# Optimization experiments

Hardware: AMD Instinct MI355X
Metric: run time of the kernel (lower is better)

The kernel has to match this reference:

```python
import jax, jax.numpy as jnp
import numpy as np

B, T, D = 2, 2048, 2048
N_HEADS, N_KV = 16, 4
HD = D // N_HEADS  # 128
ROPE_BASE = 10000.0


def _rope_tables(t, dim, base=ROPE_BASE):
    inv_freq = 1.0 / (base ** (jnp.arange(0, dim, 2, dtype=jnp.float32) / dim))
    freqs = jnp.arange(t, dtype=jnp.float32)[:, None] * inv_freq[None, :]  # (T, dim/2)
    emb = jnp.concatenate([freqs, freqs], axis=-1)  # (T, dim)
    return jnp.cos(emb), jnp.sin(emb)


def _rotate_half(x):
    x1, x2 = jnp.split(x, 2, axis=-1)
    return jnp.concatenate([-x2, x1], axis=-1)


def _apply_rope(x, cos, sin):
    # x: (B, H, T, hd); cos/sin: (T, hd)
    return x * cos[None, None] + _rotate_half(x) * sin[None, None]


def setup_inputs() -> dict:
    key = jax.random.key(0)
    ks = jax.random.split(key, 5)
    s = 0.02
    return {
        "x": jax.random.normal(ks[0], (B, T, D), jnp.float32),
        "wq": jax.random.normal(ks[1], (D, N_HEADS * HD), jnp.float32) * s,
        "wk": jax.random.normal(ks[2], (D, N_KV * HD), jnp.float32) * s,
        "wv": jax.random.normal(ks[3], (D, N_KV * HD), jnp.float32) * s,
        "wo": jax.random.normal(ks[4], (D, D), jnp.float32) * s,
    }


def reference(x, wq, wk, wv, wo):
    b, t, c = x.shape
    n_rep = N_HEADS // N_KV
    scale = 1.0 / np.sqrt(HD)

    q = (x @ wq).reshape(b, t, N_HEADS, HD).transpose(0, 2, 1, 3)  # (B,H,T,hd)
    k = (x @ wk).reshape(b, t, N_KV, HD).transpose(0, 2, 1, 3)     # (B,Hkv,T,hd)
    v = (x @ wv).reshape(b, t, N_KV, HD).transpose(0, 2, 1, 3)

    cos, sin = _rope_tables(t, HD)
    q = _apply_rope(q, cos, sin)
    k = _apply_rope(k, cos, sin)

    # repeat_kv (GQA)
    k = jnp.repeat(k, n_rep, axis=1)  # (B,H,T,hd)
    v = jnp.repeat(v, n_rep, axis=1)

    scores = jnp.einsum("bhqd,bhkd->bhqk", q, k) * scale
    causal = jnp.tril(jnp.ones((t, t), dtype=bool))
    scores = jnp.where(causal[None, None], scores, -jnp.inf)
    attn = jax.nn.softmax(scores, axis=-1)
    out = jnp.einsum("bhqk,bhkd->bhqd", attn, v)
    out = out.transpose(0, 2, 1, 3).reshape(b, t, c)
    return out @ wo
```

## Files before the change

kernel.cpp:

```cpp
#include <hip/hip_runtime.h>
#include <hip/hip_bf16.h>
#include <math.h>

#define B_   2
#define T_   2048
#define D_   2048
#define NH_  16
#define NKV_ 4
#define HD_  128
#define MROWS (B_*T_)
#define NQKV  (NH_*HD_ + 2*NKV_*HD_)

typedef __bf16 bf16_t;
typedef __bf16 bf16x8 __attribute__((ext_vector_type(8)));
typedef __bf16 bf16x4 __attribute__((ext_vector_type(4)));
typedef float  floatx4 __attribute__((ext_vector_type(4)));

__device__ __forceinline__ void async_copy16(const bf16_t* gsrc, bf16_t* ldst) {
  __builtin_amdgcn_global_load_lds(
      (const __attribute__((address_space(1))) unsigned int*)gsrc,
      (__attribute__((address_space(3))) unsigned int*)ldst, 16, 0, 0);
}

__global__ void prep_fused(const float* __restrict__ s0, const float* __restrict__ s1,
                           const float* __restrict__ s2, const float* __restrict__ s3,
                           const float* __restrict__ sx,
                           bf16_t* __restrict__ d0, bf16_t* __restrict__ d1,
                           bf16_t* __restrict__ d2, bf16_t* __restrict__ d3,
                           bf16_t* __restrict__ dx) {
  const int z = blockIdx.z;
  const int tx = threadIdx.x, ty = threadIdx.y;
  if (z == 4) {
    int i = ((blockIdx.y * 64 + blockIdx.x) * 256 + ty * 32 + tx) * 8;
    float4 a = *(const float4*)(sx + i);
    float4 b = *(const float4*)(sx + i + 4);
    bf16x8 v;
    v[0]=(bf16_t)a.x; v[1]=(bf16_t)a.y; v[2]=(bf16_t)a.z; v[3]=(bf16_t)a.w;
    v[4]=(bf16_t)b.x; v[5]=(bf16_t)b.y; v[6]=(bf16_t)b.z; v[7]=(bf16_t)b.w;
    *(bf16x8*)(dx + i) = v;
    return;
  }
  const int N = (z == 1 || z == 2) ? 512 : 2048;
  const int n0 = blockIdx.x * 32;
  if (n0 >= N) return;
  const float* src = (z == 0) ? s0 : (z == 1) ? s1 : (z == 2) ? s2 : s3;
  bf16_t*      dst = (z == 0) ? d0 : (z == 1) ? d1 : (z == 2) ? d2 : d3;
  const int K = 2048;
  __shared__ float tile[32][33];
  int k0 = blockIdx.y * 32;
#pragma unroll
  for (int r = 0; r < 4; r++)
    tile[ty + r*8][tx] = src[(size_t)(k0 + ty + r*8) * N + n0 + tx];
  __syncthreads();
#pragma unroll
  for (int r = 0; r < 4; r++)
    dst[(size_t)(n0 + ty + r*8) * K + k0 + tx] = (bf16_t)tile[tx][ty + r*8];
}

template <typename OUT_T>
__global__ __launch_bounds__(256, 3)
void gemm_bt(const bf16_t* __restrict__ A, const bf16_t* __restrict__ Bt,
             OUT_T* __restrict__ C, int M, int N, int K) {
  __shared__ __align__(16) bf16_t As[128 * 64];
  __shared__ __align__(16) bf16_t Bs[128 * 64];
  const int tid  = threadIdx.x;
  const int wave = tid >> 6, lane = tid & 63;
  const int quad = lane >> 4, l16 = lane & 15;
  const int nBlocksM = M >> 7;
  const int bm = blockIdx.x % nBlocksM, bn = blockIdx.x / nBlocksM;
  const int m0 = bm * 128, n0 = bn * 128;
  const int wm = (wave >> 1) * 64, wn = (wave & 1) * 64;

  floatx4 acc[4][4];
#pragma unroll
  for (int i = 0; i < 4; i++)
#pragma unroll
    for (int j = 0; j < 4; j++) acc[i][j] = floatx4{0.f, 0.f, 0.f, 0.f};

  for (int k0 = 0; k0 < K; k0 += 64) {
    __syncthreads();
#pragma unroll
    for (int i = 0; i < 4; i++) {
      int e = i * 256 + tid;
      int row = e >> 3, grp = e & 7;
      int gg = grp ^ (row & 7);
      async_copy16(A + (size_t)(m0 + row) * K + k0 + gg * 8, As + e * 8);
    }
#pragma unroll
    for (int i = 0; i < 4; i++) {
      int e = i * 256 + tid;
      int row = e >> 3, grp = e & 7;
      int gg = grp ^ (row & 7);
      async_copy16(Bt + (size_t)(n0 + row) * K + k0 + gg * 8, Bs + e * 8);
    }
    __syncthreads();
#pragma unroll
    for (int ks = 0; ks < 2; ks++) {
      bf16x8 af[4], bfr[4];
      int grp = ks * 4 + quad;
#pragma unroll
      for (int mi = 0; mi < 4; mi++) {
        int row = wm + mi * 16 + l16;
        af[mi] = *(const bf16x8*)(As + row * 64 + ((grp ^ (row & 7)) << 3));
      }
#pragma unroll
      for (int ni = 0; ni < 4; ni++) {
        int row = wn + ni * 16 + l16;
        bfr[ni] = *(const bf16x8*)(Bs + row * 64 + ((grp ^ (row & 7)) << 3));
      }
#pragma unroll
      for (int mi = 0; mi < 4; mi++)
#pragma unroll
        for (int ni = 0; ni < 4; ni++)
          acc[mi][ni] = __builtin_amdgcn_mfma_f32_16x16x32_bf16(af[mi], bfr[ni], acc[mi][ni], 0, 0, 0);
    }
  }
#pragma unroll
  for (int mi = 0; mi < 4; mi++) {
#pragma unroll
    for (int r = 0; r < 4; r++) {
      int row = m0 + wm + mi * 16 + quad * 4 + r;
      size_t base = (size_t)row * N + n0 + wn;
#pragma unroll
      for (int ni = 0; ni < 4; ni++)
        C[base + ni * 16 + l16] = (OUT_T)acc[mi][ni][r];
    }
  }
}

#define ROPE_BLOCKS ((MROWS * NKV_ * 64) / 256)
__global__ void kv_prep(const bf16_t* __restrict__ qkv, bf16_t* __restrict__ Kb,
                        bf16_t* __restrict__ Vt) {
  if (blockIdx.x < ROPE_BLOCKS) {
    int g = blockIdx.x * 256 + threadIdx.x;
    int j = g & 63;
    int rest = g >> 6;
    int kvh = rest & 3;
    int row = rest >> 2;
    int t = row & (T_ - 1);
    int b = row >> 11;
    const bf16_t* src = qkv + (size_t)row * NQKV + NH_ * HD_ + kvh * HD_;
    float ang = (float)t * __expf(-0.14391156816f * (float)j);
    float sn, cs;
    __sincosf(ang, &sn, &cs);
    float x0 = (float)src[j];
    float x1 = (float)src[j + 64];
    bf16_t* dst = Kb + ((size_t)(b * NKV_ + kvh) * T_ + t) * HD_;
    dst[j]      = (bf16_t)(x0 * cs - x1 * sn);
    dst[j + 64] = (bf16_t)(x1 * cs + x0 * sn);
    return;
  }
  __shared__ float tile[32][33];
  int bb = blockIdx.x - ROPE_BLOCKS;
  int bx = bb & 63, by = (bb >> 6) & 3, bz = bb >> 8;
  int t0 = bx * 32, d0 = by * 32;
  int b = bz / NKV_, kvh = bz % NKV_;
  int tx = threadIdx.x & 31, ty = threadIdx.x >> 5;
#pragma unroll
  for (int r = 0; r < 4; r++) {
    int t = t0 + ty + r * 8;
    tile[ty + r*8][tx] =
        (float)qkv[(size_t)(b * T_ + t) * NQKV + (NH_ + NKV_) * HD_ + kvh * HD_ + d0 + tx];
  }
  __syncthreads();
#pragma unroll
  for (int r = 0; r < 4; r++) {
    int d = d0 + ty + r * 8;
    Vt[((size_t)(b * NKV_ + kvh) * HD_ + d) * T_ + t0 + tx] = (bf16_t)tile[tx][ty + r*8];
  }
}

__global__ __launch_bounds__(256, 2)
void flash_attn(const bf16_t* __restrict__ qkv, const bf16_t* __restrict__ Kb,
                const bf16_t* __restrict__ Vt, bf16_t* __restrict__ Ob) {
  __shared__ __align__(16) bf16_t Ks[2][64 * 128];
  __shared__ __align__(16) bf16_t Vs[2][128 * 64];

  const int tid = threadIdx.x;
  const int wave = tid >> 6, lane = tid & 63;
  const int quad = lane >> 4, l16 = lane & 15;
  const int nQT = T_ / 64;
  const int bid = blockIdx.x;
  const int bh = bid % (B_ * NH_);
  const int qt = (nQT - 1) - (bid / (B_ * NH_));
  const int h = bh % NH_;
  const int b = bh / NH_;
  const int kv = h >> 2;

  const bf16_t* kbase = Kb + ((size_t)(b * NKV_ + kv) * T_) * HD_;
  const bf16_t* vbase = Vt + ((size_t)(b * NKV_ + kv) * HD_) * T_;

  auto stage = [&](int kt, int bufi) {
#pragma unroll
    for (int i = 0; i < 4; i++) {
      int e = i * 256 + tid;
      int row = e >> 4, grp = e & 15;
      int gg = grp ^ (row & 15);
      async_copy16(kbase + (size_t)(kt * 64 + row) * HD_ + gg * 8, &Ks[bufi][e * 8]);
    }
#pragma unroll
    for (int i = 0; i < 4; i++) {
      int e = i * 256 + tid;
      int row = e >> 3, grp = e & 7;
      int gg = grp ^ (row & 7);
      async_copy16(vbase + (size_t)row * T_ + kt * 64 + gg * 8, &Vs[bufi][e * 8]);
    }
  };

  stage(0, 0);

  bf16x8 qf[4];
  {
    const int t_row = qt * 64 + wave * 16 + l16;
    const bf16_t* qptr = qkv + (size_t)(b * T_ + t_row) * NQKV + h * HD_;
    bf16x8 qraw[4];
#pragma unroll
    for (int ks = 0; ks < 4; ks++)
      qraw[ks] = *(const bf16x8*)(qptr + ks * 32 + quad * 8);
    const float scale = 0.12751651541057752f;
#pragma unroll
    for (int ks = 0; ks < 2; ks++)
#pragma unroll
      for (int j = 0; j < 8; j++) {
        int d = ks * 32 + quad * 8 + j;
        float ang = (float)t_row * __expf(-0.14391156816f * (float)d);
        float sn, cs;
        __sincosf(ang, &sn, &cs);
        float lo = (float)qraw[ks][j], hi = (float)qraw[ks + 2][j];
        qf[ks][j]     = (bf16_t)((lo * cs - hi * sn) * scale);
        qf[ks + 2][j] = (bf16_t)((hi * cs + lo * sn) * scale);
      }
  }

  floatx4 o[8];
#pragma unroll
  for (int i = 0; i < 8; i++) o[i] = floatx4{0.f, 0.f, 0.f, 0.f};
  float m_s = -1e30f, l_s = 0.f;

  for (int kt = 0; kt <= qt; kt++) {
    const int bufi = kt & 1;
    __syncthreads();
    if (kt < qt) stage(kt + 1, bufi ^ 1);

    floatx4 s[4];
#pragma unroll
    for (int nt = 0; nt < 4; nt++) s[nt] = floatx4{0.f, 0.f, 0.f, 0.f};
    __builtin_amdgcn_s_setprio(1);
#pragma unroll
    for (int ks = 0; ks < 4; ks++) {
      int grp = ks * 4 + quad;
#pragma unroll
      for (int nt = 0; nt < 4; nt++) {
        int row = nt * 16 + l16;
        bf16x8 kf = *(const bf16x8*)(&Ks[bufi][row * 128 + ((grp ^ (row & 15)) << 3)]);
        s[nt] = __builtin_amdgcn_mfma_f32_16x16x32_bf16(kf, qf[ks], s[nt], 0, 0, 0);
      }
    }
    __builtin_amdgcn_s_setprio(0);

    if (kt == qt) {
      int qlocal = wave * 16 + l16;
#pragma unroll
      for (int nt = 0; nt < 4; nt++)
#pragma unroll
        for (int r = 0; r < 4; r++) {
          int klocal = nt * 16 + quad * 4 + r;
          if (klocal > qlocal) s[nt][r] = -1e30f;
        }
    }

    float mx = fmaxf(fmaxf(s[0][0], s[0][1]), fmaxf(s[0][2], s[0][3]));
#pragma unroll
    for (int nt = 1; nt < 4; nt++)
      mx = fmaxf(mx, fmaxf(fmaxf(s[nt][0], s[nt][1]), fmaxf(s[nt][2], s[nt][3])));
    mx = fmaxf(mx, __shfl_xor(mx, 16, 64));
    mx = fmaxf(mx, __shfl_xor(mx, 32, 64));
    if (!__all(mx <= m_s + 8.0f)) {
      float mnew = fmaxf(m_s, mx);
      float alpha = __builtin_amdgcn_exp2f(m_s - mnew);
      m_s = mnew;
      l_s *= alpha;
#pragma unroll
      for (int dt = 0; dt < 8; dt++) o[dt] *= alpha;
    }
    float sum = 0.f;
#pragma unroll
    for (int nt = 0; nt < 4; nt++)
#pragma unroll
      for (int r = 0; r < 4; r++) {
        float p = __builtin_amdgcn_exp2f(s[nt][r] - m_s);
        s[nt][r] = p;
        sum += p;
      }
    sum += __shfl_xor(sum, 16, 64);
    sum += __shfl_xor(sum, 32, 64);
    l_s += sum;

    __builtin_amdgcn_s_setprio(1);
#pragma unroll
    for (int ks = 0; ks < 2; ks++) {
      bf16x8 pf;
#pragma unroll
      for (int j = 0; j < 4; j++) {
        pf[j]     = (bf16_t)s[ks][j];
        pf[j + 4] = (bf16_t)s[ks + 2][j];
      }
      const int glo = 2 * ks + (quad >> 1);
      const int ghi = glo + 4;
      const int half = (quad & 1) * 4;
#pragma unroll
      for (int dt = 0; dt < 8; dt++) {
        int row = dt * 16 + l16;
        int sw = row & 7;
        const bf16_t* vrow = &Vs[bufi][row * 64];
        bf16x4 vlo = *(const bf16x4*)(vrow + (((glo ^ sw) << 3) + half));
        bf16x4 vhi = *(const bf16x4*)(vrow + (((ghi ^ sw) << 3) + half));
        bf16x8 vf = __builtin_shufflevector(vlo, vhi, 0, 1, 2, 3, 4, 5, 6, 7);
        o[dt] = __builtin_amdgcn_mfma_f32_16x16x32_bf16(vf, pf, o[dt], 0, 0, 0);
      }
    }
    __builtin_amdgcn_s_setprio(0);
  }

  {
    int qg = qt * 64 + wave * 16 + l16;
    float inv_l = 1.f / l_s;
    size_t base = ((size_t)(b * T_) + qg) * D_ + h * HD_;
#pragma unroll
    for (int dt = 0; dt < 8; dt++) {
      bf16x4 w;
#pragma unroll
      for (int r = 0; r < 4; r++) w[r] = (bf16_t)(o[dt][r] * inv_l);
      *(bf16x4*)(Ob + base + dt * 16 + quad * 4) = w;
    }
  }
}

extern "C" void kernel_launch(void* const* d_in, const int* in_sizes, int n_in,
                              void* d_out, int out_size, void* d_ws, size_t ws_size,
                              hipStream_t stream) {
  const float* x  = (const float*)d_in[0];
  const float* wq = (const float*)d_in[1];
  const float* wk = (const float*)d_in[2];
  const float* wv = (const float*)d_in[3];
  const float* wo = (const float*)d_in[4];
  float* out = (float*)d_out;

  bf16_t* x_bf   = (bf16_t*)d_ws;
  bf16_t* attn_o = x_bf;
  bf16_t* wqkv_t = x_bf + (size_t)MROWS * D_;
  bf16_t* wo_t   = wqkv_t + (size_t)NQKV * D_;
  bf16_t* qkv    = wo_t + (size_t)D_ * D_;
  bf16_t* Kb     = qkv + (size_t)MROWS * NQKV;
  bf16_t* Vt     = Kb + (size_t)B_ * NKV_ * T_ * HD_;

  prep_fused<<<dim3(64, 64, 5), dim3(32, 8), 0, stream>>>(
      wq, wk, wv, wo, x,
      wqkv_t, wqkv_t + (size_t)2048 * D_, wqkv_t + (size_t)2560 * D_, wo_t, x_bf);

  gemm_bt<bf16_t><<<(MROWS / 128) * (NQKV / 128), 256, 0, stream>>>(
      x_bf, wqkv_t, qkv, MROWS, NQKV, D_);

  kv_prep<<<ROPE_BLOCKS + (T_ / 32) * (HD_ / 32) * B_ * NKV_, 256, 0, stream>>>(
      qkv, Kb, Vt);

  flash_attn<<<B_ * NH_ * (T_ / 64), 256, 0, stream>>>(qkv, Kb, Vt, attn_o);

  gemm_bt<float><<<(MROWS / 128) * (D_ / 128), 256, 0, stream>>>(
      attn_o, wo_t, out, MROWS, D_, D_);
}
```

Measured before the change: 286.0 us.

## Process two query tiles per flash-attention block and pre-permute V layout

Each flash-attention workgroup now handles 128 query rows as two 64-row groups, so every K/V tile staged into LDS feeds twice as many MFMAs and global K/V traffic is halved. The V transpose in kv_prep writes keys in a permuted order so the PV MFMA operand can be read with one 16-byte LDS load instead of two 8-byte loads plus a shuffle. The grid is halved and the block order pairs long and short causal tiles. The cost is doubled accumulator and score register pressure under launch_bounds(256,2), which may cause spills or lower occupancy, plus some extra masked work on the last two key tiles.

```diff
diff --git a/kernel.cpp b/kernel.cpp
--- a/kernel.cpp
+++ b/kernel.cpp
@@ -166,7 +166,11 @@
 #pragma unroll
   for (int r = 0; r < 4; r++) {
     int d = d0 + ty + r * 8;
-    Vt[((size_t)(b * NKV_ + kvh) * HD_ + d) * T_ + t0 + tx] = (bf16_t)tile[tx][ty + r*8];
+    int t = t0 + tx;
+    int k = t & 63;
+    int pos = ((((k >> 4) & 1) * 4 + ((k >> 2) & 3)) << 3) + ((k >> 5) << 2) + (k & 3);
+    Vt[((size_t)(b * NKV_ + kvh) * HD_ + d) * T_ + (t & ~63) + pos] =
+        (bf16_t)tile[tx][ty + r*8];
   }
 }
 
@@ -179,13 +183,15 @@
   const int tid = threadIdx.x;
   const int wave = tid >> 6, lane = tid & 63;
   const int quad = lane >> 4, l16 = lane & 15;
-  const int nQT = T_ / 64;
   const int bid = blockIdx.x;
-  const int bh = bid % (B_ * NH_);
-  const int qt = (nQT - 1) - (bid / (B_ * NH_));
-  const int h = bh % NH_;
-  const int b = bh / NH_;
+  const int bh = bid & 31;
+  const int qtp = bid >> 5;
+  const int qt2 = (qtp < 8) ? (15 - qtp) : (qtp - 8);
+  const int h = bh & 15;
+  const int b = bh >> 4;
   const int kv = h >> 2;
+  const int q0 = qt2 * 128;
+  const int ktLast = 2 * qt2 + 1;
 
   const bf16_t* kbase = Kb + ((size_t)(b * NKV_ + kv) * T_) * HD_;
   const bf16_t* vbase = Vt + ((size_t)(b * NKV_ + kv) * HD_) * T_;
@@ -209,9 +215,10 @@
 
   stage(0, 0);
 
-  bf16x8 qf[4];
-  {
-    const int t_row = qt * 64 + wave * 16 + l16;
+  bf16x8 qf[2][4];
+#pragma unroll
+  for (int g = 0; g < 2; g++) {
+    const int t_row = q0 + g * 64 + wave * 16 + l16;
     const bf16_t* qptr = qkv + (size_t)(b * T_ + t_row) * NQKV + h * HD_;
     bf16x8 qraw[4];
 #pragma unroll
@@ -227,24 +234,30 @@
         float sn, cs;
         __sincosf(ang, &sn, &cs);
         float lo = (float)qraw[ks][j], hi = (float)qraw[ks + 2][j];
-        qf[ks][j]     = (bf16_t)((lo * cs - hi * sn) * scale);
-        qf[ks + 2][j] = (bf16_t)((hi * cs + lo * sn) * scale);
-      }
-  }
-
-  floatx4 o[8];
-#pragma unroll
-  for (int i = 0; i < 8; i++) o[i] = floatx4{0.f, 0.f, 0.f, 0.f};
-  float m_s = -1e30f, l_s = 0.f;
-
-  for (int kt = 0; kt <= qt; kt++) {
+        qf[g][ks][j]     = (bf16_t)((lo * cs - hi * sn) * scale);
+        qf[g][ks + 2][j] = (bf16_t)((hi * cs + lo * sn) * scale);
+      }
+  }
+
+  floatx4 o[2][8];
+#pragma unroll
+  for (int g = 0; g < 2; g++)
+#pragma unroll
+    for (int i = 0; i < 8; i++) o[g][i] = floatx4{0.f, 0.f, 0.f, 0.f};
+  float m_s[2] = {-1e30f, -1e30f}, l_s[2] = {0.f, 0.f};
+
+  const int qlocal64 = wave * 16 + l16;
+
+  for (int kt = 0; kt <= ktLast; kt++) {
     const int bufi = kt & 1;
     __syncthreads();
-    if (kt < qt) stage(kt + 1, bufi ^ 1);
-
-    floatx4 s[4];
-#pragma unroll
-    for (int nt = 0; nt < 4; nt++) s[nt] = floatx4{0.f, 0.f, 0.f, 0.f};
+    if (kt < ktLast) stage(kt + 1, bufi ^ 1);
+
+    floatx4 s[2][4];
+#pragma unroll
+    for (int g = 0; g < 2; g++)
+#pragma unroll
+      for (int nt = 0; nt < 4; nt++) s[g][nt] = floatx4{0.f, 0.f, 0.f, 0.f};
     __builtin_amdgcn_s_setprio(1);
 #pragma unroll
     for (int ks = 0; ks < 4; ks++) {
@@ -253,84 +266,91 @@
       for (int nt = 0; nt < 4; nt++) {
         int row = nt * 16 + l16;
         bf16x8 kf = *(const bf16x8*)(&Ks[bufi][row * 128 + ((grp ^ (row & 15)) << 3)]);
-        s[nt] = __builtin_amdgcn_mfma_f32_16x16x32_bf16(kf, qf[ks], s[nt], 0, 0, 0);
+        s[0][nt] = __builtin_amdgcn_mfma_f32_16x16x32_bf16(kf, qf[0][ks], s[0][nt], 0, 0, 0);
+        s[1][nt] = __builtin_amdgcn_mfma_f32_16x16x32_bf16(kf, qf[1][ks], s[1][nt], 0, 0, 0);
       }
     }
     __builtin_amdgcn_s_setprio(0);
 
-    if (kt == qt) {
-      int qlocal = wave * 16 + l16;
+#pragma unroll
+    for (int g = 0; g < 2; g++) {
+      int ktd = 2 * qt2 + g;
+      if (kt >= ktd) {
+        int koff = (kt - ktd) * 64;
+#pragma unroll
+        for (int nt = 0; nt < 4; nt++)
+#pragma unroll
+          for (int r = 0; r < 4; r++) {
+            int klocal = nt * 16 + quad * 4 + r + koff;
+            if (klocal > qlocal64) s[g][nt][r] = -1e30f;
+          }
+      }
+    }
+
+#pragma unroll
+    for (int g = 0; g < 2; g++) {
+      float mx = fmaxf(fmaxf(s[g][0][0], s[g][0][1]), fmaxf(s[g][0][2], s[g][0][3]));
+#pragma unroll
+      for (int nt = 1; nt < 4; nt++)
+        mx = fmaxf(mx, fmaxf(fmaxf(s[g][nt][0], s[g][nt][1]),
+                             fmaxf(s[g][nt][2], s[g][nt][3])));
+      mx = fmaxf(mx, __shfl_xor(mx, 16, 64));
+      mx = fmaxf(mx, __shfl_xor(mx, 32, 64));
+      if (!__all(mx <= m_s[g] + 8.0f)) {
+        float mnew = fmaxf(m_s[g], mx);
+        float alpha = __builtin_amdgcn_exp2f(m_s[g] - mnew);
+        m_s[g] = mnew;
+        l_s[g] *= alpha;
+#pragma unroll
+        for (int dt = 0; dt < 8; dt++) o[g][dt] *= alpha;
+      }
+      float sum = 0.f;
 #pragma unroll
       for (int nt = 0; nt < 4; nt++)
 #pragma unroll
         for (int r = 0; r < 4; r++) {
-          int klocal = nt * 16 + quad * 4 + r;
-          if (klocal > qlocal) s[nt][r] = -1e30f;
+          float p = __builtin_amdgcn_exp2f(s[g][nt][r] - m_s[g]);
+          s[g][nt][r] = p;
+          sum += p;
         }
-    }
-
-    float mx = fmaxf(fmaxf(s[0][0], s[0][1]), fmaxf(s[0][2], s[0][3]));
-#pragma unroll
-    for (int nt = 1; nt < 4; nt++)
-      mx = fmaxf(mx, fmaxf(fmaxf(s[nt][0], s[nt][1]), fmaxf(s[nt][2], s[nt][3])));
-    mx = fmaxf(mx, __shfl_xor(mx, 16, 64));
-    mx = fmaxf(mx, __shfl_xor(mx, 32, 64));
-    if (!__all(mx <= m_s + 8.0f)) {
-      float mnew = fmaxf(m_s, mx);
-      float alpha = __builtin_amdgcn_exp2f(m_s - mnew);
-      m_s = mnew;
-      l_s *= alpha;
-#pragma unroll
-      for (int dt = 0; dt < 8; dt++) o[dt] *= alpha;
-    }
-    float sum = 0.f;
-#pragma unroll
-    for (int nt = 0; nt < 4; nt++)
-#pragma unroll
-      for (int r = 0; r < 4; r++) {
-        float p = __builtin_amdgcn_exp2f(s[nt][r] - m_s);
-        s[nt][r] = p;
-        sum += p;
-      }
-    sum += __shfl_xor(sum, 16, 64);
-    sum += __shfl_xor(sum, 32, 64);
-    l_s += sum;
+      sum += __shfl_xor(sum, 16, 64);
+      sum += __shfl_xor(sum, 32, 64);
+      l_s[g] += sum;
+    }
 
     __builtin_amdgcn_s_setprio(1);
 #pragma unroll
     for (int ks = 0; ks < 2; ks++) {
-      bf16x8 pf;
+      bf16x8 pf0, pf1;
 #pragma unroll
       for (int j = 0; j < 4; j++) {
-        pf[j]     = (bf16_t)s[ks][j];
-        pf[j + 4] = (bf16_t)s[ks + 2][j];
-      }
-      const int glo = 2 * ks + (quad >> 1);
-      const int ghi = glo + 4;
-      const int half = (quad & 1) * 4;
+        pf0[j]     = (bf16_t)s[0][ks][j];
+        pf0[j + 4] = (bf16_t)s[0][ks + 2][j];
+        pf1[j]     = (bf16_t)s[1][ks][j];
+        pf1[j + 4] = (bf16_t)s[1][ks + 2][j];
+      }
+      const int G = ks * 4 + quad;
 #pragma unroll
       for (int dt = 0; dt < 8; dt++) {
         int row = dt * 16 + l16;
-        int sw = row & 7;
-        const bf16_t* vrow = &Vs[bufi][row * 64];
-        bf16x4 vlo = *(const bf16x4*)(vrow + (((glo ^ sw) << 3) + half));
-        bf16x4 vhi = *(const bf16x4*)(vrow + (((ghi ^ sw) << 3) + half));
-        bf16x8 vf = __builtin_shufflevector(vlo, vhi, 0, 1, 2, 3, 4, 5, 6, 7);
-        o[dt] = __builtin_amdgcn_mfma_f32_16x16x32_bf16(vf, pf, o[dt], 0, 0, 0);
+        bf16x8 vf = *(const bf16x8*)(&Vs[bufi][row * 64 + ((G ^ (row & 7)) << 3)]);
+        o[0][dt] = __builtin_amdgcn_mfma_f32_16x16x32_bf16(vf, pf0, o[0][dt], 0, 0, 0);
+        o[1][dt] = __builtin_amdgcn_mfma_f32_16x16x32_bf16(vf, pf1, o[1][dt], 0, 0, 0);
       }
     }
     __builtin_amdgcn_s_setprio(0);
   }
 
-  {
-    int qg = qt * 64 + wave * 16 + l16;
-    float inv_l = 1.f / l_s;
+#pragma unroll
+  for (int g = 0; g < 2; g++) {
+    int qg = q0 + g * 64 + wave * 16 + l16;
+    float inv_l = 1.f / l_s[g];
     size_t base = ((size_t)(b * T_) + qg) * D_ + h * HD_;
 #pragma unroll
     for (int dt = 0; dt < 8; dt++) {
       bf16x4 w;
 #pragma unroll
-      for (int r = 0; r < 4; r++) w[r] = (bf16_t)(o[dt][r] * inv_l);
+      for (int r = 0; r < 4; r++) w[r] = (bf16_t)(o[g][dt][r] * inv_l);
       *(bf16x4*)(Ob + base + dt * 16 + quad * 4) = w;
     }
   }
@@ -364,7 +384,7 @@
   kv_prep<<<ROPE_BLOCKS + (T_ / 32) * (HD_ / 32) * B_ * NKV_, 256, 0, stream>>>(
       qkv, Kb, Vt);
 
-  flash_attn<<<B_ * NH_ * (T_ / 64), 256, 0, stream>>>(qkv, Kb, Vt, attn_o);
+  flash_attn<<<B_ * NH_ * (T_ / 128), 256, 0, stream>>>(qkv, Kb, Vt, attn_o);
 
   gemm_bt<float><<<(MROWS / 128) * (D_ / 128), 256, 0, stream>>>(
       attn_o, wo_t, out, MROWS, D_, D_);
```

Result: no change. 284.4 us (-0.6%).

## Use 128-row query blocks sharing K/V tiles and pre-permute V layout

Applied to the files above, without the earlier changes.

Flash attention blocks now cover 128 query rows with 8 waves, so each staged K/V tile in LDS serves twice as many queries and staging per thread is halved. Work order is remapped so heavy and light causal tiles interleave. V is written in a permuted order during kv_prep so the PV step reads one 16-byte LDS vector instead of two 8-byte pieces plus a shuffle. The cost is that the lower-half waves sit idle on the final key tile, and the larger blocks may lower occupancy.

```diff
diff --git a/kernel.cpp b/kernel.cpp
--- a/kernel.cpp
+++ b/kernel.cpp
@@ -166,11 +166,15 @@
 #pragma unroll
   for (int r = 0; r < 4; r++) {
     int d = d0 + ty + r * 8;
-    Vt[((size_t)(b * NKV_ + kvh) * HD_ + d) * T_ + t0 + tx] = (bf16_t)tile[tx][ty + r*8];
-  }
-}
-
-__global__ __launch_bounds__(256, 2)
+    int t = t0 + tx;
+    int k = t & 63;
+    int pos = ((((k >> 4) & 1) * 4 + ((k >> 2) & 3)) << 3) + ((k >> 5) << 2) + (k & 3);
+    Vt[((size_t)(b * NKV_ + kvh) * HD_ + d) * T_ + (t & ~63) + pos] =
+        (bf16_t)tile[tx][ty + r*8];
+  }
+}
+
+__global__ __launch_bounds__(512, 4)
 void flash_attn(const bf16_t* __restrict__ qkv, const bf16_t* __restrict__ Kb,
                 const bf16_t* __restrict__ Vt, bf16_t* __restrict__ Ob) {
   __shared__ __align__(16) bf16_t Ks[2][64 * 128];
@@ -179,28 +183,32 @@
   const int tid = threadIdx.x;
   const int wave = tid >> 6, lane = tid & 63;
   const int quad = lane >> 4, l16 = lane & 15;
-  const int nQT = T_ / 64;
   const int bid = blockIdx.x;
-  const int bh = bid % (B_ * NH_);
-  const int qt = (nQT - 1) - (bid / (B_ * NH_));
-  const int h = bh % NH_;
-  const int b = bh / NH_;
+  const int bh = bid & 31;
+  const int p  = bid >> 5;
+  const int qm = (p < 8) ? (15 - p) : (p - 8);
+  const int h = bh & 15;
+  const int b = bh >> 4;
   const int kv = h >> 2;
+  const int wq = wave >> 2;
+  const int w4 = wave & 3;
+  const int qtw = 2 * qm + wq;
+  const int ktLast = 2 * qm + 1;
 
   const bf16_t* kbase = Kb + ((size_t)(b * NKV_ + kv) * T_) * HD_;
   const bf16_t* vbase = Vt + ((size_t)(b * NKV_ + kv) * HD_) * T_;
 
   auto stage = [&](int kt, int bufi) {
 #pragma unroll
-    for (int i = 0; i < 4; i++) {
-      int e = i * 256 + tid;
+    for (int i = 0; i < 2; i++) {
+      int e = i * 512 + tid;
       int row = e >> 4, grp = e & 15;
       int gg = grp ^ (row & 15);
       async_copy16(kbase + (size_t)(kt * 64 + row) * HD_ + gg * 8, &Ks[bufi][e * 8]);
     }
 #pragma unroll
-    for (int i = 0; i < 4; i++) {
-      int e = i * 256 + tid;
+    for (int i = 0; i < 2; i++) {
+      int e = i * 512 + tid;
       int row = e >> 3, grp = e & 7;
       int gg = grp ^ (row & 7);
       async_copy16(vbase + (size_t)row * T_ + kt * 64 + gg * 8, &Vs[bufi][e * 8]);
@@ -211,7 +219,7 @@
 
   bf16x8 qf[4];
   {
-    const int t_row = qt * 64 + wave * 16 + l16;
+    const int t_row = qtw * 64 + w4 * 16 + l16;
     const bf16_t* qptr = qkv + (size_t)(b * T_ + t_row) * NQKV + h * HD_;
     bf16x8 qraw[4];
 #pragma unroll
@@ -237,93 +245,90 @@
   for (int i = 0; i < 8; i++) o[i] = floatx4{0.f, 0.f, 0.f, 0.f};
   float m_s = -1e30f, l_s = 0.f;
 
-  for (int kt = 0; kt <= qt; kt++) {
+  const int qlocal = w4 * 16 + l16;
+
+  for (int kt = 0; kt <= ktLast; kt++) {
     const int bufi = kt & 1;
     __syncthreads();
-    if (kt < qt) stage(kt + 1, bufi ^ 1);
-
-    floatx4 s[4];
-#pragma unroll
-    for (int nt = 0; nt < 4; nt++) s[nt] = floatx4{0.f, 0.f, 0.f, 0.f};
-    __builtin_amdgcn_s_setprio(1);
-#pragma unroll
-    for (int ks = 0; ks < 4; ks++) {
-      int grp = ks * 4 + quad;
-#pragma unroll
-      for (int nt = 0; nt < 4; nt++) {
-        int row = nt * 16 + l16;
-        bf16x8 kf = *(const bf16x8*)(&Ks[bufi][row * 128 + ((grp ^ (row & 15)) << 3)]);
-        s[nt] = __builtin_amdgcn_mfma_f32_16x16x32_bf16(kf, qf[ks], s[nt], 0, 0, 0);
-      }
-    }
-    __builtin_amdgcn_s_setprio(0);
-
-    if (kt == qt) {
-      int qlocal = wave * 16 + l16;
+    if (kt < ktLast) stage(kt + 1, bufi ^ 1);
+
+    if (kt <= qtw) {
+      floatx4 s[4];
+#pragma unroll
+      for (int nt = 0; nt < 4; nt++) s[nt] = floatx4{0.f, 0.f, 0.f, 0.f};
+      __builtin_amdgcn_s_setprio(1);
+#pragma unroll
+      for (int ks = 0; ks < 4; ks++) {
+        int grp = ks * 4 + quad;
+#pragma unroll
+        for (int nt = 0; nt < 4; nt++) {
+          int row = nt * 16 + l16;
+          bf16x8 kf = *(const bf16x8*)(&Ks[bufi][row * 128 + ((grp ^ (row & 15)) << 3)]);
+          s[nt] = __builtin_amdgcn_mfma_f32_16x16x32_bf16(kf, qf[ks], s[nt], 0, 0, 0);
+        }
+      }
+      __builtin_amdgcn_s_setprio(0);
+
+      if (kt == qtw) {
+#pragma unroll
+        for (int nt = 0; nt < 4; nt++)
+#pragma unroll
+          for (int r = 0; r < 4; r++) {
+            int klocal = nt * 16 + quad * 4 + r;
+            if (klocal > qlocal) s[nt][r] = -1e30f;
+          }
+      }
+
+      float mx = fmaxf(fmaxf(s[0][0], s[0][1]), fmaxf(s[0][2], s[0][3]));
+#pragma unroll
+      for (int nt = 1; nt < 4; nt++)
+        mx = fmaxf(mx, fmaxf(fmaxf(s[nt][0], s[nt][1]), fmaxf(s[nt][2], s[nt][3])));
+      mx = fmaxf(mx, __shfl_xor(mx, 16, 64));
+      mx = fmaxf(mx, __shfl_xor(mx, 32, 64));
+      if (!__all(mx <= m_s + 8.0f)) {
+        float mnew = fmaxf(m_s, mx);
+        float alpha = __builtin_amdgcn_exp2f(m_s - mnew);
+        m_s = mnew;
+        l_s *= alpha;
+#pragma unroll
+        for (int dt = 0; dt < 8; dt++) o[dt] *= alpha;
+      }
+      float sum = 0.f;
 #pragma unroll
       for (int nt = 0; nt < 4; nt++)
 #pragma unroll
         for (int r = 0; r < 4; r++) {
-          int klocal = nt * 16 + quad * 4 + r;
-          if (klocal > qlocal) s[nt][r] = -1e30f;
+          float pv = __builtin_amdgcn_exp2f(s[nt][r] - m_s);
+          s[nt][r] = pv;
+          sum += pv;
         }
-    }
-
-    float mx = fmaxf(fmaxf(s[0][0], s[0][1]), fmaxf(s[0][2], s[0][3]));
-#pragma unroll
-    for (int nt = 1; nt < 4; nt++)
-      mx = fmaxf(mx, fmaxf(fmaxf(s[nt][0], s[nt][1]), fmaxf(s[nt][2], s[nt][3])));
-    mx = fmaxf(mx, __shfl_xor(mx, 16, 64));
-    mx = fmaxf(mx, __shfl_xor(mx, 32, 64));
-    if (!__all(mx <= m_s + 8.0f)) {
-      float mnew = fmaxf(m_s, mx);
-      float alpha = __builtin_amdgcn_exp2f(m_s - mnew);
-      m_s = mnew;
-      l_s *= alpha;
-#pragma unroll
-      for (int dt = 0; dt < 8; dt++) o[dt] *= alpha;
-    }
-    float sum = 0.f;
-#pragma unroll
-    for (int nt = 0; nt < 4; nt++)
-#pragma unroll
-      for (int r = 0; r < 4; r++) {
-        float p = __builtin_amdgcn_exp2f(s[nt][r] - m_s);
-        s[nt][r] = p;
-        sum += p;
-      }
-    sum += __shfl_xor(sum, 16, 64);
-    sum += __shfl_xor(sum, 32, 64);
-    l_s += sum;
-
-    __builtin_amdgcn_s_setprio(1);
-#pragma unroll
-    for (int ks = 0; ks < 2; ks++) {
-      bf16x8 pf;
-#pragma unroll
-      for (int j = 0; j < 4; j++) {
-        pf[j]     = (bf16_t)s[ks][j];
-        pf[j + 4] = (bf16_t)s[ks + 2][j];
-      }
-      const int glo = 2 * ks + (quad >> 1);
-      const int ghi = glo + 4;
-      const int half = (quad & 1) * 4;
-#pragma unroll
-      for (int dt = 0; dt < 8; dt++) {
-        int row = dt * 16 + l16;
-        int sw = row & 7;
-        const bf16_t* vrow = &Vs[bufi][row * 64];
-        bf16x4 vlo = *(const bf16x4*)(vrow + (((glo ^ sw) << 3) + half));
-        bf16x4 vhi = *(const bf16x4*)(vrow + (((ghi ^ sw) << 3) + half));
-        bf16x8 vf = __builtin_shufflevector(vlo, vhi, 0, 1, 2, 3, 4, 5, 6, 7);
-        o[dt] = __builtin_amdgcn_mfma_f32_16x16x32_bf16(vf, pf, o[dt], 0, 0, 0);
-      }
-    }
-    __builtin_amdgcn_s_setprio(0);
+      sum += __shfl_xor(sum, 16, 64);
+      sum += __shfl_xor(sum, 32, 64);
+      l_s += sum;
+
+      __builtin_amdgcn_s_setprio(1);
+#pragma unroll
+      for (int ks = 0; ks < 2; ks++) {
+        bf16x8 pf;
+#pragma unroll
+        for (int j = 0; j < 4; j++) {
+          pf[j]     = (bf16_t)s[ks][j];
+          pf[j + 4] = (bf16_t)s[ks + 2][j];
+        }
+        const int G = ks * 4 + quad;
+#pragma unroll
+        for (int dt = 0; dt < 8; dt++) {
+          int row = dt * 16 + l16;
+          bf16x8 vf = *(const bf16x8*)(&Vs[bufi][row * 64 + ((G ^ (row & 7)) << 3)]);
+          o[dt] = __builtin_amdgcn_mfma_f32_16x16x32_bf16(vf, pf, o[dt], 0, 0, 0);
+        }
+      }
+      __builtin_amdgcn_s_setprio(0);
+    }
   }
 
   {
-    int qg = qt * 64 + wave * 16 + l16;
+    int qg = qtw * 64 + w4 * 16 + l16;
     float inv_l = 1.f / l_s;
     size_t base = ((size_t)(b * T_) + qg) * D_ + h * HD_;
 #pragma unroll
@@ -364,7 +369,7 @@
   kv_prep<<<ROPE_BLOCKS + (T_ / 32) * (HD_ / 32) * B_ * NKV_, 256, 0, stream>>>(
       qkv, Kb, Vt);
 
-  flash_attn<<<B_ * NH_ * (T_ / 64), 256, 0, stream>>>(qkv, Kb, Vt, attn_o);
+  flash_attn<<<B_ * NH_ * (T_ / 128), 512, 0, stream>>>(qkv, Kb, Vt, attn_o);
 
   gemm_bt<float><<<(MROWS / 128) * (D_ / 128), 256, 0, stream>>>(
       attn_o, wo_t, out, MROWS, D_, D_);
```

New measurement: 270.2 us. -5.6%, faster.
